# Optimization experiments

Hardware: AMD Instinct MI355X
Metric: run time of the kernel (lower is better)

## Reference

```python
import jax, jax.numpy as jnp
import numpy as np

E = 8          # num experts
H = 1024       # hidden size
I = 512        # moe intermediate size
K = 2          # top_k
B, S = 1, 2048


def setup_inputs() -> dict:
    key = jax.random.key(0)
    k1, k2, k3, k4, k5 = jax.random.split(key, 5)
    hidden_states = jax.random.normal(k1, (B, S, H), dtype=jnp.float32)
    router_indices = jax.random.randint(k2, (B * S, K), 0, E, dtype=jnp.int64)
    routing_weights = jax.random.uniform(k3, (B * S, K), dtype=jnp.float32)
    # kaiming-uniform-ish init per expert
    bound_gu = 1.0 / np.sqrt(H)
    bound_d = 1.0 / np.sqrt(I)
    gate_up_proj = jax.random.uniform(k4, (E, H, 2 * I), dtype=jnp.float32,
                                      minval=-bound_gu, maxval=bound_gu)
    down_proj = jax.random.uniform(k5, (E, I, H), dtype=jnp.float32,
                                   minval=-bound_d, maxval=bound_d)
    return {
        "hidden_states": hidden_states,
        "router_indices": router_indices,
        "routing_weights": routing_weights,
        "gate_up_proj": gate_up_proj,
        "down_proj": down_proj,
    }


def reference(hidden_states, router_indices, routing_weights, gate_up_proj, down_proj):
    b, s, h = hidden_states.shape
    x = hidden_states.reshape(b * s, h)                    # [T, H]
    # combine weights: sum over top-k slots of routing weight for each expert
    one_hot = jax.nn.one_hot(router_indices, E, dtype=x.dtype)   # [T, K, E]
    combine = jnp.einsum('tke,tk->te', one_hot, routing_weights)  # [T, E]
    # dense dispatch: every token through every expert, masked/weighted by combine
    gate_up = jnp.einsum('th,ehf->tef', x, gate_up_proj)   # [T, E, 2I]
    gate, up = jnp.split(gate_up, 2, axis=-1)              # [T, E, I] each
    inter = jax.nn.silu(gate) * up                         # SwiGLU (no limit clamp)
    out = jnp.einsum('tef,efh,te->th', inter, down_proj, combine)  # [T, H]
    return out.reshape(b, s, h)
```

## Files before the change

kernel.cpp:

```cpp
#include <hip/hip_runtime.h>
#include <stdint.h>

#define T_TOK 2048
#define H_DIM 1024
#define ID    512
#define E_NUM 8
#define NPAIR 4096
#define BM    128
#define MAXTILES 40

typedef _Float16 half_t;
typedef _Float16 f16x8 __attribute__((ext_vector_type(8)));
typedef _Float16 f16x4 __attribute__((ext_vector_type(4)));
typedef float    f32x4 __attribute__((ext_vector_type(4)));

#define XB_OFF    ((size_t)0)
#define WGU_OFF   ((size_t)(4u << 20))
#define WDN_OFF   ((size_t)(20u << 20))
#define INTER_OFF ((size_t)(28u << 20))
#define META_OFF  ((size_t)(32u << 20))
#define PAIRW_OFF ((size_t)((32u << 20) + 32768))

__device__ __forceinline__ void gload_lds16(const void* g, void* l) {
    __builtin_amdgcn_global_load_lds(
        (const __attribute__((address_space(1))) unsigned int*)g,
        (__attribute__((address_space(3))) unsigned int*)l,
        16, 0, 0);
}

#define PIPE_BARRIER(N)                                          \
    {                                                            \
        asm volatile("s_waitcnt vmcnt(" #N ")" ::: "memory");    \
        __builtin_amdgcn_s_barrier();                            \
        __builtin_amdgcn_sched_barrier(0);                       \
    }

template <int NT>
__device__ __forceinline__ void cvt_tile64(const float* __restrict__ in,
                                           half_t* __restrict__ out,
                                           int r0, int c0, int out_stride,
                                           char* smem) {
    float (*tile)[65] = (float(*)[65])smem;
    int tid = threadIdx.x;
#pragma unroll
    for (int it = 0; it < 1024 / NT; it++) {
        int idx = tid + it * NT;
        int r = idx >> 4, c4 = (idx & 15) * 4;
        float4 v = *(const float4*)(in + (size_t)(r0 + r) * 1024 + c0 + c4);
        tile[r][c4] = v.x; tile[r][c4 + 1] = v.y; tile[r][c4 + 2] = v.z; tile[r][c4 + 3] = v.w;
    }
    __syncthreads();
#pragma unroll
    for (int it = 0; it < 1024 / NT; it++) {
        int idx = tid + it * NT;
        int oc = idx >> 4, r4 = (idx & 15) * 4;
        f16x4 o;
        o[0] = (half_t)tile[r4][oc];
        o[1] = (half_t)tile[r4 + 1][oc];
        o[2] = (half_t)tile[r4 + 2][oc];
        o[3] = (half_t)tile[r4 + 3][oc];
        *(f16x4*)(out + (size_t)(c0 + oc) * out_stride + r0 + r4) = o;
    }
}

__global__ __launch_bounds__(256) void k_prep(const float* __restrict__ x,
                                              const int* __restrict__ ridx,
                                              const float* __restrict__ rw,
                                              const float* __restrict__ wgu,
                                              half_t* __restrict__ xb,
                                              half_t* __restrict__ wguT,
                                              int* __restrict__ meta,
                                              float* __restrict__ pair_w) {
    __shared__ char smem[16704];
    int b = blockIdx.x, tid = threadIdx.x;
    if (b < 1024) {
        int g = b * 256 + tid;
        size_t b0 = (size_t)g * 8;
        float4 v0 = *(const float4*)(x + b0);
        float4 v1 = *(const float4*)(x + b0 + 4);
        f16x8 o;
        o[0] = (half_t)v0.x; o[1] = (half_t)v0.y; o[2] = (half_t)v0.z; o[3] = (half_t)v0.w;
        o[4] = (half_t)v1.x; o[5] = (half_t)v1.y; o[6] = (half_t)v1.z; o[7] = (half_t)v1.w;
        *(f16x8*)(xb + b0) = o;
    } else if (b == 1024) {
        __shared__ int cnt[E_NUM], cur[E_NUM], base[E_NUM];
        if (tid < E_NUM) { cnt[tid] = 0; cur[tid] = 0; }
        __syncthreads();
        for (int i = tid; i < NPAIR; i += 256) atomicAdd(&cnt[ridx[i]], 1);
        __syncthreads();
        if (tid == 0) {
            int acc = 0, nt = 0;
            for (int e = 0; e < E_NUM; e++) {
                base[e] = acc;
                for (int r = 0; r < cnt[e]; r += BM) {
                    meta[8 + nt] = e; meta[88 + nt] = acc + r; meta[168 + nt] = acc + cnt[e]; nt++;
                }
                acc += cnt[e];
            }
            meta[0] = nt;
        }
        __syncthreads();
        for (int i = tid; i < NPAIR; i += 256) {
            int e = ridx[i];
            int pos = atomicAdd(&cur[e], 1);
            int slot = base[e] + pos;
            meta[256 + slot] = i >> 1;
            pair_w[slot] = rw[i];
        }
    } else {
        int t = b - 1025;
        int e = t >> 8, rem = t & 255;
        int h0 = (rem >> 4) * 64, f0 = (rem & 15) * 64;
        cvt_tile64<256>(wgu + (size_t)e * 1024 * 1024, wguT + (size_t)e * 1024 * 1024,
                        h0, f0, 1024, smem);
    }
}

template <int MODE>
__global__ __launch_bounds__(256) void k_gemm(const int* __restrict__ meta,
                                              const half_t* __restrict__ amat,
                                              const half_t* __restrict__ wT,
                                              const float* __restrict__ pair_w,
                                              void* __restrict__ outp,
                                              const float* __restrict__ aux_in,
                                              half_t* __restrict__ aux_out,
                                              float4* __restrict__ zero_out) {
    constexpr int KSZ = MODE ? ID : H_DIM;
    constexpr int NKT = KSZ / 32;
    __shared__ __align__(16) char smem[49152];

    int d = blockIdx.x;
    if (MODE == 0 && d >= 320) {
        int d2 = d - 320;
        if (d2 < 1024) {
            int e = d2 >> 7, rem = d2 & 127;
            int h0 = (rem >> 3) * 64, i0 = (rem & 7) * 64;
            cvt_tile64<256>(aux_in + (size_t)e * ID * 1024, aux_out + (size_t)e * 1024 * ID,
                            i0, h0, ID, smem);
        } else {
            int z = d2 - 1024;
            float4 zv = make_float4(0.f, 0.f, 0.f, 0.f);
            float4* p = zero_out + (size_t)z * 1024 + threadIdx.x;
            p[0] = zv; p[256] = zv; p[512] = zv; p[768] = zv;
        }
        return;
    }

    int l = (d & 7) * MAXTILES + (d >> 3);
    int bx = l >> 3, by = l & 7;
    int nt = meta[0];
    if (bx >= nt) return;
    int e = meta[8 + bx], row0 = meta[88 + bx], rend = meta[168 + bx];
    const int* pair_token = meta + 256;

    int tid = threadIdx.x, lane = tid & 63, wid = tid >> 6;
    int wm = wid >> 1, wn = wid & 1;

    const half_t* asrc[2]; int aoff[2];
#pragma unroll
    for (int i = 0; i < 2; i++) {
        int gch = wid * 2 + i;
        int r = gch * 16 + (lane >> 2);
        int lc = (lane & 3) ^ ((r >> 2) & 3);
        int pr = row0 + r; if (pr > NPAIR - 1) pr = NPAIR - 1;
        const half_t* rowp = (MODE == 0) ? amat + (size_t)pair_token[pr] * KSZ
                                         : amat + (size_t)pr * KSZ;
        asrc[i] = rowp + lc * 8;
        aoff[i] = gch * 1024;
    }
    const half_t* wbase = wT + (size_t)e * 1024 * KSZ;
    const half_t* bsrc[2]; int boff[2];
#pragma unroll
    for (int i = 0; i < 2; i++) {
        int gch = wid * 2 + i;
        int br = gch * 16 + (lane >> 2);
        int lc = (lane & 3) ^ ((br >> 2) & 3);
        int physcol;
        if (MODE == 0) {
            int w = br >> 6, f = (br >> 4) & 3, ll = br & 15;
            physcol = by * 64 + w * 32 + (f & 1) * 16 + ll + ((f & 2) ? 512 : 0);
        } else {
            physcol = by * 128 + br;
        }
        bsrc[i] = wbase + (size_t)physcol * KSZ + lc * 8;
        boff[i] = 8192 + gch * 1024;
    }

    auto stage = [&](int buf, int kt) {
        char* base = smem + buf * 16384;
#pragma unroll
        for (int i = 0; i < 2; i++) gload_lds16(asrc[i] + kt * 32, base + aoff[i]);
#pragma unroll
        for (int i = 0; i < 2; i++) gload_lds16(bsrc[i] + kt * 32, base + boff[i]);
    };

    f32x4 acc[4][4] = {};

    auto compute = [&](int buf) {
        const char* Ab = smem + buf * 16384;
        const char* Bb = Ab + 8192;
        f16x8 af[4], bf[4];
#pragma unroll
        for (int f = 0; f < 4; f++) {
            int ar = wm * 64 + f * 16 + (lane & 15);
            int apc = (lane >> 4) ^ ((ar >> 2) & 3);
            af[f] = *(const f16x8*)(Ab + ar * 64 + apc * 16);
            int br = wn * 64 + f * 16 + (lane & 15);
            int bpc = (lane >> 4) ^ ((br >> 2) & 3);
            bf[f] = *(const f16x8*)(Bb + br * 64 + bpc * 16);
        }
#pragma unroll
        for (int fm = 0; fm < 4; fm++)
#pragma unroll
            for (int fn = 0; fn < 4; fn++)
                acc[fm][fn] = __builtin_amdgcn_mfma_f32_16x16x32_f16(af[fm], bf[fn], acc[fm][fn], 0, 0, 0);
    };

    stage(0, 0);
    stage(1, 1);
    int cur = 0, stg = 2;
    for (int kt = 0; kt < NKT - 2; kt++) {
        PIPE_BARRIER(4);
        stage(stg, kt + 2);
        compute(cur);
        cur = cur == 2 ? 0 : cur + 1;
        stg = stg == 2 ? 0 : stg + 1;
    }
    PIPE_BARRIER(4);
    compute(cur);
    cur = cur == 2 ? 0 : cur + 1;
    PIPE_BARRIER(0);
    compute(cur);

    if (MODE == 0) {
        half_t* inter = (half_t*)outp;
#pragma unroll
        for (int fm = 0; fm < 4; fm++) {
            int rbase = wm * 64 + fm * 16 + (lane >> 4) * 4;
#pragma unroll
            for (int j = 0; j < 4; j++) {
                int packed = row0 + rbase + j;
                if (packed < rend) {
                    half_t* rowp = inter + (size_t)packed * ID;
#pragma unroll
                    for (int fn = 0; fn < 2; fn++) {
                        int col = by * 64 + wn * 32 + fn * 16 + (lane & 15);
                        float g = acc[fm][fn][j], u = acc[fm][fn + 2][j];
                        rowp[col] = (half_t)(g / (1.0f + __expf(-g)) * u);
                    }
                }
            }
        }
    } else {
        float* out = (float*)outp;
#pragma unroll
        for (int fm = 0; fm < 4; fm++) {
            int rbase = wm * 64 + fm * 16 + (lane >> 4) * 4;
#pragma unroll
            for (int j = 0; j < 4; j++) {
                int packed = row0 + rbase + j;
                if (packed < rend) {
                    int t = pair_token[packed];
                    float pw = pair_w[packed];
#pragma unroll
                    for (int fn = 0; fn < 4; fn++) {
                        int col = by * 128 + wn * 64 + fn * 16 + (lane & 15);
                        __hip_atomic_fetch_add(&out[(size_t)t * H_DIM + col],
                                               acc[fm][fn][j] * pw,
                                               __ATOMIC_RELAXED,
                                               __HIP_MEMORY_SCOPE_AGENT);
                    }
                }
            }
        }
    }
}

extern "C" void kernel_launch(void* const* d_in, const int* in_sizes, int n_in,
                              void* d_out, int out_size, void* d_ws, size_t ws_size,
                              hipStream_t stream) {
    const float* x    = (const float*)d_in[0];
    const int*   ridx = (const int*)d_in[1];
    const float* rw   = (const float*)d_in[2];
    const float* wgu  = (const float*)d_in[3];
    const float* wdn  = (const float*)d_in[4];
    float* out = (float*)d_out;

    char* ws = (char*)d_ws;
    half_t* xb    = (half_t*)(ws + XB_OFF);
    half_t* wguT  = (half_t*)(ws + WGU_OFF);
    half_t* wdnT  = (half_t*)(ws + WDN_OFF);
    half_t* inter = (half_t*)(ws + INTER_OFF);
    int*    meta  = (int*)(ws + META_OFF);
    float*  pair_w = (float*)(ws + PAIRW_OFF);

    k_prep<<<3073, 256, 0, stream>>>(x, ridx, rw, wgu, xb, wguT, meta, pair_w);
    k_gemm<0><<<1856, 256, 0, stream>>>(meta, xb, wguT, pair_w, inter, wdn, wdnT, (float4*)out);
    k_gemm<1><<<320, 256, 0, stream>>>(meta, inter, wdnT, pair_w, out, nullptr, nullptr, nullptr);
}
```

Baseline: 69.14 us.

## Shrink GEMM tiles to 64x64 with a 128-wide K step and double buffering

Both expert GEMMs move from 128x128 output tiles with a 32-wide K step and a 3-stage pipeline to 64x64 tiles with a 128-wide K step, a 16-slot XOR swizzle and a 2-buffer pipeline synchronised with __syncthreads. Tile metadata and grid mapping grow to 72 row tiles times 16 column tiles. The aim is more workgroups to fill the CUs and less padding waste per expert segment. In exchange, each tile reuses less data, the LDS footprint grows to 64KB, and the finer-grained vmcnt-based overlap from the old 3-stage pipeline is lost.

```diff
diff --git a/kernel.cpp b/kernel.cpp
--- a/kernel.cpp
+++ b/kernel.cpp
@@ -6,8 +6,9 @@
 #define ID    512
 #define E_NUM 8
 #define NPAIR 4096
-#define BM    128
-#define MAXTILES 40
+#define BM    64
+#define MAXTILES 72
+#define NGRID1   1152
 
 typedef _Float16 half_t;
 typedef _Float16 f16x8 __attribute__((ext_vector_type(8)));
@@ -27,13 +28,6 @@
         (__attribute__((address_space(3))) unsigned int*)l,
         16, 0, 0);
 }
-
-#define PIPE_BARRIER(N)                                          \
-    {                                                            \
-        asm volatile("s_waitcnt vmcnt(" #N ")" ::: "memory");    \
-        __builtin_amdgcn_s_barrier();                            \
-        __builtin_amdgcn_sched_barrier(0);                       \
-    }
 
 template <int NT>
 __device__ __forceinline__ void cvt_tile64(const float* __restrict__ in,
@@ -126,12 +120,12 @@
                                               half_t* __restrict__ aux_out,
                                               float4* __restrict__ zero_out) {
     constexpr int KSZ = MODE ? ID : H_DIM;
-    constexpr int NKT = KSZ / 32;
-    __shared__ __align__(16) char smem[49152];
+    constexpr int NKT = KSZ / 128;
+    __shared__ __align__(16) char smem[65536];
 
     int d = blockIdx.x;
-    if (MODE == 0 && d >= 320) {
-        int d2 = d - 320;
+    if (MODE == 0 && d >= NGRID1) {
+        int d2 = d - NGRID1;
         if (d2 < 1024) {
             int e = d2 >> 7, rem = d2 & 127;
             int h0 = (rem >> 3) * 64, i0 = (rem & 7) * 64;
@@ -146,8 +140,8 @@
         return;
     }
 
-    int l = (d & 7) * MAXTILES + (d >> 3);
-    int bx = l >> 3, by = l & 7;
+    int l = (d & 7) * 144 + (d >> 3);
+    int bx = l >> 4, by = l & 15;
     int nt = meta[0];
     if (bx >= nt) return;
     int e = meta[8 + bx], row0 = meta[88 + bx], rend = meta[168 + bx];
@@ -156,12 +150,12 @@
     int tid = threadIdx.x, lane = tid & 63, wid = tid >> 6;
     int wm = wid >> 1, wn = wid & 1;
 
-    const half_t* asrc[2]; int aoff[2];
-#pragma unroll
-    for (int i = 0; i < 2; i++) {
-        int gch = wid * 2 + i;
-        int r = gch * 16 + (lane >> 2);
-        int lc = (lane & 3) ^ ((r >> 2) & 3);
+    const half_t* asrc[4]; int aoff[4];
+#pragma unroll
+    for (int i = 0; i < 4; i++) {
+        int gch = wid * 4 + i;
+        int r = gch * 4 + (lane >> 4);
+        int lc = (lane & 15) ^ (r & 15);
         int pr = row0 + r; if (pr > NPAIR - 1) pr = NPAIR - 1;
         const half_t* rowp = (MODE == 0) ? amat + (size_t)pair_token[pr] * KSZ
                                          : amat + (size_t)pr * KSZ;
@@ -169,93 +163,86 @@
         aoff[i] = gch * 1024;
     }
     const half_t* wbase = wT + (size_t)e * 1024 * KSZ;
-    const half_t* bsrc[2]; int boff[2];
-#pragma unroll
-    for (int i = 0; i < 2; i++) {
-        int gch = wid * 2 + i;
-        int br = gch * 16 + (lane >> 2);
-        int lc = (lane & 3) ^ ((br >> 2) & 3);
+    const half_t* bsrc[4]; int boff[4];
+#pragma unroll
+    for (int i = 0; i < 4; i++) {
+        int gch = wid * 4 + i;
+        int nr = gch * 4 + (lane >> 4);
+        int lc = (lane & 15) ^ (nr & 15);
         int physcol;
         if (MODE == 0) {
-            int w = br >> 6, f = (br >> 4) & 3, ll = br & 15;
-            physcol = by * 64 + w * 32 + (f & 1) * 16 + ll + ((f & 2) ? 512 : 0);
+            int w = nr >> 5, f = (nr >> 4) & 1, ll = nr & 15;
+            physcol = by * 32 + w * 16 + ll + (f ? 512 : 0);
         } else {
-            physcol = by * 128 + br;
+            physcol = by * 64 + nr;
         }
         bsrc[i] = wbase + (size_t)physcol * KSZ + lc * 8;
-        boff[i] = 8192 + gch * 1024;
+        boff[i] = 16384 + gch * 1024;
     }
 
     auto stage = [&](int buf, int kt) {
-        char* base = smem + buf * 16384;
-#pragma unroll
-        for (int i = 0; i < 2; i++) gload_lds16(asrc[i] + kt * 32, base + aoff[i]);
-#pragma unroll
-        for (int i = 0; i < 2; i++) gload_lds16(bsrc[i] + kt * 32, base + boff[i]);
+        char* base = smem + buf * 32768;
+#pragma unroll
+        for (int i = 0; i < 4; i++) gload_lds16(asrc[i] + kt * 128, base + aoff[i]);
+#pragma unroll
+        for (int i = 0; i < 4; i++) gload_lds16(bsrc[i] + kt * 128, base + boff[i]);
     };
 
-    f32x4 acc[4][4] = {};
+    f32x4 acc[2][2] = {};
 
     auto compute = [&](int buf) {
-        const char* Ab = smem + buf * 16384;
-        const char* Bb = Ab + 8192;
-        f16x8 af[4], bf[4];
-#pragma unroll
-        for (int f = 0; f < 4; f++) {
-            int ar = wm * 64 + f * 16 + (lane & 15);
-            int apc = (lane >> 4) ^ ((ar >> 2) & 3);
-            af[f] = *(const f16x8*)(Ab + ar * 64 + apc * 16);
-            int br = wn * 64 + f * 16 + (lane & 15);
-            int bpc = (lane >> 4) ^ ((br >> 2) & 3);
-            bf[f] = *(const f16x8*)(Bb + br * 64 + bpc * 16);
-        }
-#pragma unroll
-        for (int fm = 0; fm < 4; fm++)
-#pragma unroll
-            for (int fn = 0; fn < 4; fn++)
-                acc[fm][fn] = __builtin_amdgcn_mfma_f32_16x16x32_f16(af[fm], bf[fn], acc[fm][fn], 0, 0, 0);
+        const char* Ab = smem + buf * 32768;
+        const char* Bb = Ab + 16384;
+#pragma unroll
+        for (int ks = 0; ks < 4; ks++) {
+            f16x8 af[2], bf[2];
+#pragma unroll
+            for (int f = 0; f < 2; f++) {
+                int ar = wm * 32 + f * 16 + (lane & 15);
+                int aslot = (ks * 4 + (lane >> 4)) ^ (ar & 15);
+                af[f] = *(const f16x8*)(Ab + ar * 256 + aslot * 16);
+                int br = wn * 32 + f * 16 + (lane & 15);
+                int bslot = (ks * 4 + (lane >> 4)) ^ (br & 15);
+                bf[f] = *(const f16x8*)(Bb + br * 256 + bslot * 16);
+            }
+#pragma unroll
+            for (int fm = 0; fm < 2; fm++)
+#pragma unroll
+                for (int fn = 0; fn < 2; fn++)
+                    acc[fm][fn] = __builtin_amdgcn_mfma_f32_16x16x32_f16(af[fm], bf[fn], acc[fm][fn], 0, 0, 0);
+        }
     };
 
     stage(0, 0);
-    stage(1, 1);
-    int cur = 0, stg = 2;
-    for (int kt = 0; kt < NKT - 2; kt++) {
-        PIPE_BARRIER(4);
-        stage(stg, kt + 2);
+    __syncthreads();
+    int cur = 0;
+    for (int kt = 0; kt < NKT; kt++) {
+        if (kt + 1 < NKT) stage(cur ^ 1, kt + 1);
         compute(cur);
-        cur = cur == 2 ? 0 : cur + 1;
-        stg = stg == 2 ? 0 : stg + 1;
-    }
-    PIPE_BARRIER(4);
-    compute(cur);
-    cur = cur == 2 ? 0 : cur + 1;
-    PIPE_BARRIER(0);
-    compute(cur);
+        __syncthreads();
+        cur ^= 1;
+    }
 
     if (MODE == 0) {
         half_t* inter = (half_t*)outp;
 #pragma unroll
-        for (int fm = 0; fm < 4; fm++) {
-            int rbase = wm * 64 + fm * 16 + (lane >> 4) * 4;
+        for (int fm = 0; fm < 2; fm++) {
+            int rbase = wm * 32 + fm * 16 + (lane >> 4) * 4;
 #pragma unroll
             for (int j = 0; j < 4; j++) {
                 int packed = row0 + rbase + j;
                 if (packed < rend) {
-                    half_t* rowp = inter + (size_t)packed * ID;
-#pragma unroll
-                    for (int fn = 0; fn < 2; fn++) {
-                        int col = by * 64 + wn * 32 + fn * 16 + (lane & 15);
-                        float g = acc[fm][fn][j], u = acc[fm][fn + 2][j];
-                        rowp[col] = (half_t)(g / (1.0f + __expf(-g)) * u);
-                    }
+                    int col = by * 32 + wn * 16 + (lane & 15);
+                    float g = acc[fm][0][j], u = acc[fm][1][j];
+                    inter[(size_t)packed * ID + col] = (half_t)(g / (1.0f + __expf(-g)) * u);
                 }
             }
         }
     } else {
         float* out = (float*)outp;
 #pragma unroll
-        for (int fm = 0; fm < 4; fm++) {
-            int rbase = wm * 64 + fm * 16 + (lane >> 4) * 4;
+        for (int fm = 0; fm < 2; fm++) {
+            int rbase = wm * 32 + fm * 16 + (lane >> 4) * 4;
 #pragma unroll
             for (int j = 0; j < 4; j++) {
                 int packed = row0 + rbase + j;
@@ -263,8 +250,8 @@
                     int t = pair_token[packed];
                     float pw = pair_w[packed];
 #pragma unroll
-                    for (int fn = 0; fn < 4; fn++) {
-                        int col = by * 128 + wn * 64 + fn * 16 + (lane & 15);
+                    for (int fn = 0; fn < 2; fn++) {
+                        int col = by * 64 + wn * 32 + fn * 16 + (lane & 15);
                         __hip_atomic_fetch_add(&out[(size_t)t * H_DIM + col],
                                                acc[fm][fn][j] * pw,
                                                __ATOMIC_RELAXED,
@@ -295,6 +282,6 @@
     float*  pair_w = (float*)(ws + PAIRW_OFF);
 
     k_prep<<<3073, 256, 0, stream>>>(x, ridx, rw, wgu, xb, wguT, meta, pair_w);
-    k_gemm<0><<<1856, 256, 0, stream>>>(meta, xb, wguT, pair_w, inter, wdn, wdnT, (float4*)out);
-    k_gemm<1><<<320, 256, 0, stream>>>(meta, inter, wdnT, pair_w, out, nullptr, nullptr, nullptr);
-}
+    k_gemm<0><<<NGRID1 + 1536, 256, 0, stream>>>(meta, xb, wguT, pair_w, inter, wdn, wdnT, (float4*)out);
+    k_gemm<1><<<NGRID1, 256, 0, stream>>>(meta, inter, wdnT, pair_w, out, nullptr, nullptr, nullptr);
+}
```

Result: slower. 76.37 us (+10.5%).
